# Kernel tuning notes

Hardware: AMD Instinct MI355X
Metric: run time of the kernel (lower is better)

The kernel has to match this reference:

```python
import jax, jax.numpy as jnp
import numpy as np

EPS = 1e-10
COMMITMENT_COST = 0.25


def setup_inputs() -> dict:
    key = jax.random.key(0)
    k1, k2 = jax.random.split(key)
    inputs = jax.random.normal(k1, (64, 64, 32, 32), dtype=jnp.float32)
    # nn.init.uniform_(weight, -1.0, 1.0)
    embeddings = jax.random.uniform(k2, (1024, 64), dtype=jnp.float32, minval=-1.0, maxval=1.0)
    return {"inputs": inputs, "embeddings": embeddings}


def reference(inputs, embeddings):
    B, C, H, W = inputs.shape  # C == embedding_dim
    K = embeddings.shape[0]
    x = jnp.transpose(inputs, (0, 2, 3, 1)).reshape(-1, C)  # [N, D]
    d = (jnp.sum(x * x, axis=1, keepdims=True)
         - 2.0 * (x @ embeddings.T)
         + jnp.sum(embeddings * embeddings, axis=1))  # [N, K]
    idx = jnp.argmin(d, axis=1)  # [N]
    # one-hot @ embeddings == gather
    q = jnp.take(embeddings, idx, axis=0)  # [N, D]
    x4 = x.reshape(B, H, W, C)
    q4 = q.reshape(B, H, W, C)
    e_latent = jnp.mean((jax.lax.stop_gradient(q4) - x4) ** 2)
    q_latent = jnp.mean((q4 - jax.lax.stop_gradient(x4)) ** 2)
    loss = q_latent + COMMITMENT_COST * e_latent
    # straight-through estimator
    st = x4 + jax.lax.stop_gradient(q4 - x4)
    # avg_probs = mean of one-hot encodings == normalized histogram
    n = idx.shape[0]
    avg_probs = jnp.zeros((K,), dtype=jnp.float32).at[idx].add(1.0) / n
    perplexity = jnp.exp(-jnp.sum(avg_probs * jnp.log(avg_probs + EPS)))
    quantized = jnp.transpose(st, (0, 3, 1, 2))
    return quantized, loss, perplexity
```

## Files before the change

kernel.cpp:

```cpp
#include <hip/hip_runtime.h>

#define N_TOTAL   65536
#define HW_SZ     1024
#define CDIM      64
#define K_CODES   1024
#define OUT_ELEMS 4194304
#define QT        256
#define NCHUNK    4
#define TAU       0.004f


typedef __attribute__((ext_vector_type(8))) short short8;
typedef __attribute__((ext_vector_type(4))) float f32x4;

__device__ __forceinline__ unsigned short f2bf(float x) {
    unsigned u = __float_as_uint(x);
    return (unsigned short)((u + 0x7FFFu + ((u >> 16) & 1u)) >> 16);
}
__device__ __forceinline__ float bf2f(unsigned short h) {
    return __uint_as_float(((unsigned)h) << 16);
}
__device__ __forceinline__ void gload_lds16(const void* g, void* l) {
    __builtin_amdgcn_global_load_lds(
        (const __attribute__((address_space(1))) void*)g,
        (__attribute__((address_space(3))) void*)l, 16, 0, 0);
}

__global__ void k_prep(const float* __restrict__ emb, float* __restrict__ enorm,
                       short* __restrict__ btab, unsigned int* __restrict__ hist) {
    int gid = blockIdx.x * 256 + threadIdx.x;
    int r  = gid >> 4;
    int d0 = (gid & 15) * 4;
    float4 v = *(const float4*)(emb + gid * 4);
    float s = v.x * v.x + v.y * v.y + v.z * v.z + v.w * v.w;
#pragma unroll
    for (int off = 1; off < 16; off <<= 1) s += __shfl_xor(s, off, 64);
    if ((gid & 15) == 0) enorm[r] = s;

    float vv[4] = {v.x, v.y, v.z, v.w};
    short h[4], l[4];
#pragma unroll
    for (int j = 0; j < 4; ++j) {
        unsigned short hh = f2bf(vv[j]);
        h[j] = (short)hh;
        l[j] = (short)f2bf(vv[j] - bf2f(hh));
    }
    int base = (r >> 4) * 2048 + (d0 >> 5) * 1024
             + ((((d0 >> 3) & 3) * 16 + (r & 15)) * 8) + (d0 & 7);
    *(short4*)&btab[base]       = make_short4(h[0], h[1], h[2], h[3]);
    *(short4*)&btab[base + 512] = make_short4(l[0], l[1], l[2], l[3]);

    if (gid < K_CODES) hist[gid] = 0u;
}

__global__ __launch_bounds__(1024, 1)
void k_argmin(const float* __restrict__ x, const float* __restrict__ emb,
              const short* __restrict__ btab, const float* __restrict__ enorm,
              unsigned int* __restrict__ hist, float* __restrict__ partials,
              float* __restrict__ out) {
    __shared__ __align__(16) short bufs[2][16 * 2048];
    __shared__ __align__(16) float ens[K_CODES];
    __shared__ float xnorm[QT];
    __shared__ float rd1[QT];
    __shared__ float rd2[QT];
    __shared__ int   ri[QT];
    __shared__ int   flist[QT];
    __shared__ __align__(16) float xqf[CDIM];
    __shared__ float wdd[16];
    __shared__ int   wii[16];
    __shared__ float spw[4];
    __shared__ int   nflag;
    float* tile = (float*)bufs;

    const int tid  = threadIdx.x;
    const int lane = tid & 63;
    const int w    = tid >> 6;
    const int quad = lane >> 4;
    const int col  = lane & 15;

    const int n0  = blockIdx.x * QT;
    const int b   = n0 >> 10;
    const int hw0 = n0 & 1023;

    auto stage_async = [&](int c, int bsel) {
        const short* src = btab + c * (16 * 2048);
#pragma unroll
        for (int i = 0; i < 4; ++i) {
            int idx = i * 1024 + tid;
            gload_lds16(&src[idx * 8], (void*)&bufs[bsel][idx * 8]);
        }
    };

    stage_async(0, 0);
    if (tid < 256) gload_lds16(&enorm[tid * 4], (void*)&ens[tid * 4]);

    const float* xb = x + b * (CDIM * HW_SZ) + hw0 + w * 16 + col;
    short8 afr[2][2];
    float nloc = 0.f;
#pragma unroll
    for (int kc = 0; kc < 2; ++kc) {
#pragma unroll
        for (int j = 0; j < 8; ++j) {
            int c0 = (kc * 4 + quad) * 8 + j;
            float v = xb[c0 * HW_SZ];
            unsigned short hh = f2bf(v);
            afr[kc][0][j] = (short)hh;
            afr[kc][1][j] = (short)f2bf(v - bf2f(hh));
            nloc = __builtin_fmaf(v, v, nloc);
        }
    }
    nloc += __shfl_xor(nloc, 16, 64);
    nloc += __shfl_xor(nloc, 32, 64);
    if (quad == 0) xnorm[w * 16 + col] = nloc;

    float d1[4], d2[4];
    int   i1[4];
#pragma unroll
    for (int t = 0; t < 4; ++t) { d1[t] = 3.4e38f; d2[t] = 3.4e38f; i1[t] = 0; }

    __syncthreads();

    for (int c = 0; c < NCHUNK; ++c) {
        if (c + 1 < NCHUNK) stage_async(c + 1, (c + 1) & 1);
        const short* bs = &bufs[c & 1][0];
        const int cbase = c * 256;

        short8 Ba[4], Bb[4];
        float  ena, enb;
        auto LDB = [&](short8 (&B)[4], float& en, int ctl) {
            const short* fp = bs + ctl * 2048 + lane * 8;
            B[0] = *(const short8*)(fp);
            B[1] = *(const short8*)(fp + 512);
            B[2] = *(const short8*)(fp + 1024);
            B[3] = *(const short8*)(fp + 1536);
            en   = ens[cbase + ctl * 16 + col];
        };
        auto COMP = [&](const short8 (&B)[4], float en, int mycode) {
            f32x4 a0 = {0.f, 0.f, 0.f, 0.f};
            f32x4 a1 = {0.f, 0.f, 0.f, 0.f};
            a0 = __builtin_amdgcn_mfma_f32_16x16x32_bf16(afr[0][1], B[0], a0, 0, 0, 0);
            a1 = __builtin_amdgcn_mfma_f32_16x16x32_bf16(afr[1][1], B[2], a1, 0, 0, 0);
            a0 = __builtin_amdgcn_mfma_f32_16x16x32_bf16(afr[0][0], B[1], a0, 0, 0, 0);
            a1 = __builtin_amdgcn_mfma_f32_16x16x32_bf16(afr[1][0], B[3], a1, 0, 0, 0);
            a0 = __builtin_amdgcn_mfma_f32_16x16x32_bf16(afr[0][0], B[0], a0, 0, 0, 0);
            a1 = __builtin_amdgcn_mfma_f32_16x16x32_bf16(afr[1][0], B[2], a1, 0, 0, 0);
#pragma unroll
            for (int reg = 0; reg < 4; ++reg) {
                float dot = a0[reg] + a1[reg];
                float d   = __builtin_fmaf(dot, -2.f, en);
                float d1o = d1[reg];
                d2[reg] = __builtin_amdgcn_fmed3f(d, d1o, d2[reg]);
                d1[reg] = fminf(d, d1o);
                i1[reg] = (d < d1o) ? mycode : i1[reg];
            }
        };

        LDB(Ba, ena, 0);
#pragma unroll
        for (int ctl = 0; ctl < 16; ctl += 2) {
            LDB(Bb, enb, ctl + 1);
            COMP(Ba, ena, cbase + ctl * 16 + col);
            if (ctl + 2 < 16) LDB(Ba, ena, ctl + 2);
            COMP(Bb, enb, cbase + (ctl + 1) * 16 + col);
        }
        __syncthreads();
    }

#pragma unroll
    for (int t = 0; t < 4; ++t) {
        float a1 = d1[t], a2 = d2[t];
        int ai = i1[t];
#pragma unroll
        for (int off = 1; off < 16; off <<= 1) {
            float o1 = __shfl_xor(a1, off, 64);
            float o2 = __shfl_xor(a2, off, 64);
            int   oi = __shfl_xor(ai, off, 64);
            if (o1 < a1 || (o1 == a1 && oi < ai)) {
                float loser = a1; a2 = fminf(fminf(a2, o2), loser); a1 = o1; ai = oi;
            } else {
                a2 = fminf(fminf(a2, o2), o1);
            }
        }
        d1[t] = a1; d2[t] = a2; i1[t] = ai;
    }

    if (tid == 0) nflag = 0;
    if (col == 0) {
#pragma unroll
        for (int reg = 0; reg < 4; ++reg) {
            int m = w * 16 + quad * 4 + reg;
            rd1[m] = d1[reg];
            rd2[m] = d2[reg];
            ri [m] = i1[reg];
        }
    }
    __syncthreads();

    if (tid < QT) {
        if (rd2[tid] - rd1[tid] < TAU) {
            int slot = atomicAdd(&nflag, 1);
            flist[slot] = tid;
        }
    }
    __syncthreads();

    for (int f = 0; f < nflag; ++f) {
        const int q = flist[f];
        if (tid < CDIM) xqf[tid] = x[b * (CDIM * HW_SZ) + tid * HW_SZ + hw0 + q];
        __syncthreads();
        const int k = tid;
        const float4* er = (const float4*)(emb + k * CDIM);
        const float4* xr = (const float4*)xqf;
        float dot = 0.f;
#pragma unroll 4
        for (int c4 = 0; c4 < 16; ++c4) {
            float4 e = er[c4], xv = xr[c4];
            dot += e.x * xv.x + e.y * xv.y + e.z * xv.z + e.w * xv.w;
        }
        float dm = ens[k] - 2.f * dot;
        int   im = k;
#pragma unroll
        for (int off = 1; off < 64; off <<= 1) {
            float od = __shfl_xor(dm, off, 64);
            int   oi = __shfl_xor(im, off, 64);
            if (od < dm || (od == dm && oi < im)) { dm = od; im = oi; }
        }
        if (lane == 0) { wdd[w] = dm; wii[w] = im; }
        __syncthreads();
        if (tid == 0) {
            float bd = wdd[0]; int bi = wii[0];
#pragma unroll
            for (int ww = 1; ww < 16; ++ww)
                if (wdd[ww] < bd || (wdd[ww] == bd && wii[ww] < bi)) { bd = wdd[ww]; bi = wii[ww]; }
            rd1[q] = bd; ri[q] = bi;
        }
        __syncthreads();
    }

    if (tid < QT) {
        int ai = ri[tid];
        atomicAdd(&hist[ai], 1u);
        float sp = rd1[tid] + xnorm[tid];
#pragma unroll
        for (int off = 32; off; off >>= 1) sp += __shfl_down(sp, off, 64);
        if (lane == 0) spw[tid >> 6] = sp;
    }
    __syncthreads();
    if (tid == 0) partials[blockIdx.x] = spw[0] + spw[1] + spw[2] + spw[3];

#pragma unroll
    for (int h = 0; h < 4; ++h) {
        {
            int q = tid >> 4, j4 = tid & 15;
            int code = ri[h * 64 + q];
            float4 e = *(const float4*)(emb + code * CDIM + j4 * 4);
            *(float4*)&tile[q * 73 + j4 * 4] = e;
        }
        __syncthreads();
        {
            int c = tid >> 4, s = tid & 15;
            int q = s * 4;
            float4 v;
            v.x = tile[(q + 0) * 73 + c];
            v.y = tile[(q + 1) * 73 + c];
            v.z = tile[(q + 2) * 73 + c];
            v.w = tile[(q + 3) * 73 + c];
            *(float4*)&out[b * (CDIM * HW_SZ) + c * HW_SZ + hw0 + h * 64 + q] = v;
        }
        if (h < 3) __syncthreads();
    }
}

__global__ void k_final(const float* __restrict__ partials,
                        const unsigned int* __restrict__ hist,
                        float* __restrict__ out) {
    int tid = threadIdx.x;
    float ss = partials[tid];
    float s = 0.f;
#pragma unroll
    for (int i = 0; i < 4; ++i) {
        float p = (float)hist[i * 256 + tid] * (1.0f / 65536.0f);
        s += p * logf(p + 1e-10f);
    }
    __shared__ float fin[8];
#pragma unroll
    for (int off = 32; off; off >>= 1) {
        ss += __shfl_down(ss, off, 64);
        s  += __shfl_down(s, off, 64);
    }
    if ((tid & 63) == 0) { fin[tid >> 6] = ss; fin[4 + (tid >> 6)] = s; }
    __syncthreads();
    if (tid == 0) {
        float sse = fin[0] + fin[1] + fin[2] + fin[3];
        float ent = fin[4] + fin[5] + fin[6] + fin[7];
        out[OUT_ELEMS]     = 1.25f * sse * (1.0f / (float)OUT_ELEMS);
        out[OUT_ELEMS + 1] = expf(-ent);
    }
}

extern "C" void kernel_launch(void* const* d_in, const int* in_sizes, int n_in,
                              void* d_out, int out_size, void* d_ws, size_t ws_size,
                              hipStream_t stream) {
    const float* x   = (const float*)d_in[0];
    const float* emb = (const float*)d_in[1];
    float* out = (float*)d_out;
    char* ws = (char*)d_ws;
    float*        enorm    = (float*)(ws);
    unsigned int* hist     = (unsigned int*)(ws + 4096);
    float*        partials = (float*)(ws + 8192);
    short*        btab     = (short*)(ws + 12288);

    k_prep  <<<64, 256, 0, stream>>>(emb, enorm, btab, hist);
    k_argmin<<<N_TOTAL / QT, 1024, 0, stream>>>(x, emb, btab, enorm, hist, partials, out);
    k_final <<<1, 256, 0, stream>>>(partials, hist, out);
}
```

Measured before the change: 153.9 us.

## Halve argmin block to 128 queries with 512 threads and two blocks per CU

Each argmin block now handles 128 query vectors with 512 threads instead of 256 with 1024. The codebook is streamed in 8 chunks of 128 codes so each block's LDS footprint halves and two blocks can co-reside per CU. The grid doubles to 512 blocks, which spreads work across the 256 CUs and lets one block's barriers and fallback loop overlap with another's compute. In exchange, each block re-streams the full codebook for fewer queries, doubling total codebook traffic, and the exact-recheck and output-transpose loops are re-indexed for the smaller block.

```diff
diff --git a/kernel.cpp b/kernel.cpp
--- a/kernel.cpp
+++ b/kernel.cpp
@@ -5,8 +5,8 @@
 #define CDIM      64
 #define K_CODES   1024
 #define OUT_ELEMS 4194304
-#define QT        256
-#define NCHUNK    4
+#define QT        128
+#define NCHUNK    8
 #define TAU       0.004f
 
 
@@ -53,12 +53,12 @@
     if (gid < K_CODES) hist[gid] = 0u;
 }
 
-__global__ __launch_bounds__(1024, 1)
+__global__ __launch_bounds__(512, 2)
 void k_argmin(const float* __restrict__ x, const float* __restrict__ emb,
               const short* __restrict__ btab, const float* __restrict__ enorm,
               unsigned int* __restrict__ hist, float* __restrict__ partials,
               float* __restrict__ out) {
-    __shared__ __align__(16) short bufs[2][16 * 2048];
+    __shared__ __align__(16) short bufs[2][8 * 2048];
     __shared__ __align__(16) float ens[K_CODES];
     __shared__ float xnorm[QT];
     __shared__ float rd1[QT];
@@ -66,9 +66,9 @@
     __shared__ int   ri[QT];
     __shared__ int   flist[QT];
     __shared__ __align__(16) float xqf[CDIM];
-    __shared__ float wdd[16];
-    __shared__ int   wii[16];
-    __shared__ float spw[4];
+    __shared__ float wdd[8];
+    __shared__ int   wii[8];
+    __shared__ float spw[2];
     __shared__ int   nflag;
     float* tile = (float*)bufs;
 
@@ -83,10 +83,10 @@
     const int hw0 = n0 & 1023;
 
     auto stage_async = [&](int c, int bsel) {
-        const short* src = btab + c * (16 * 2048);
+        const short* src = btab + c * (8 * 2048);
 #pragma unroll
         for (int i = 0; i < 4; ++i) {
-            int idx = i * 1024 + tid;
+            int idx = i * 512 + tid;
             gload_lds16(&src[idx * 8], (void*)&bufs[bsel][idx * 8]);
         }
     };
@@ -123,7 +123,7 @@
     for (int c = 0; c < NCHUNK; ++c) {
         if (c + 1 < NCHUNK) stage_async(c + 1, (c + 1) & 1);
         const short* bs = &bufs[c & 1][0];
-        const int cbase = c * 256;
+        const int cbase = c * 128;
 
         short8 Ba[4], Bb[4];
         float  ena, enb;
@@ -157,10 +157,10 @@
 
         LDB(Ba, ena, 0);
 #pragma unroll
-        for (int ctl = 0; ctl < 16; ctl += 2) {
+        for (int ctl = 0; ctl < 8; ctl += 2) {
             LDB(Bb, enb, ctl + 1);
             COMP(Ba, ena, cbase + ctl * 16 + col);
-            if (ctl + 2 < 16) LDB(Ba, ena, ctl + 2);
+            if (ctl + 2 < 8) LDB(Ba, ena, ctl + 2);
             COMP(Bb, enb, cbase + (ctl + 1) * 16 + col);
         }
         __syncthreads();
@@ -208,17 +208,20 @@
         const int q = flist[f];
         if (tid < CDIM) xqf[tid] = x[b * (CDIM * HW_SZ) + tid * HW_SZ + hw0 + q];
         __syncthreads();
-        const int k = tid;
-        const float4* er = (const float4*)(emb + k * CDIM);
-        const float4* xr = (const float4*)xqf;
-        float dot = 0.f;
+        float dm = 3.4e38f; int im = 0;
+        for (int cd = 0; cd < 2; ++cd) {
+            const int k = tid + cd * 512;
+            const float4* er = (const float4*)(emb + k * CDIM);
+            const float4* xr = (const float4*)xqf;
+            float dot = 0.f;
 #pragma unroll 4
-        for (int c4 = 0; c4 < 16; ++c4) {
-            float4 e = er[c4], xv = xr[c4];
-            dot += e.x * xv.x + e.y * xv.y + e.z * xv.z + e.w * xv.w;
-        }
-        float dm = ens[k] - 2.f * dot;
-        int   im = k;
+            for (int c4 = 0; c4 < 16; ++c4) {
+                float4 e = er[c4], xv = xr[c4];
+                dot += e.x * xv.x + e.y * xv.y + e.z * xv.z + e.w * xv.w;
+            }
+            float d = ens[k] - 2.f * dot;
+            if (d < dm) { dm = d; im = k; }
+        }
 #pragma unroll
         for (int off = 1; off < 64; off <<= 1) {
             float od = __shfl_xor(dm, off, 64);
@@ -230,7 +233,7 @@
         if (tid == 0) {
             float bd = wdd[0]; int bi = wii[0];
 #pragma unroll
-            for (int ww = 1; ww < 16; ++ww)
+            for (int ww = 1; ww < 8; ++ww)
                 if (wdd[ww] < bd || (wdd[ww] == bd && wii[ww] < bi)) { bd = wdd[ww]; bi = wii[ww]; }
             rd1[q] = bd; ri[q] = bi;
         }
@@ -246,28 +249,35 @@
         if (lane == 0) spw[tid >> 6] = sp;
     }
     __syncthreads();
-    if (tid == 0) partials[blockIdx.x] = spw[0] + spw[1] + spw[2] + spw[3];
-
-#pragma unroll
-    for (int h = 0; h < 4; ++h) {
+    if (tid == 0) partials[blockIdx.x] = spw[0] + spw[1];
+
+#pragma unroll
+    for (int h = 0; h < 2; ++h) {
         {
-            int q = tid >> 4, j4 = tid & 15;
+            int q = tid >> 3, j8 = tid & 7;
             int code = ri[h * 64 + q];
-            float4 e = *(const float4*)(emb + code * CDIM + j4 * 4);
-            *(float4*)&tile[q * 73 + j4 * 4] = e;
+            const float4* er = (const float4*)(emb + code * CDIM + j8 * 8);
+            float4 e0 = er[0], e1 = er[1];
+            float* dst = &tile[q * 73 + j8 * 8];
+            *(float4*)&dst[0] = e0;
+            *(float4*)&dst[4] = e1;
         }
         __syncthreads();
         {
-            int c = tid >> 4, s = tid & 15;
-            int q = s * 4;
-            float4 v;
-            v.x = tile[(q + 0) * 73 + c];
-            v.y = tile[(q + 1) * 73 + c];
-            v.z = tile[(q + 2) * 73 + c];
-            v.w = tile[(q + 3) * 73 + c];
-            *(float4*)&out[b * (CDIM * HW_SZ) + c * HW_SZ + hw0 + h * 64 + q] = v;
-        }
-        if (h < 3) __syncthreads();
+            int c = tid >> 3;
+            float* ob = out + b * (CDIM * HW_SZ) + c * HW_SZ + hw0 + h * 64;
+#pragma unroll
+            for (int p = 0; p < 2; ++p) {
+                int q = ((tid & 7) + p * 8) * 4;
+                float4 v;
+                v.x = tile[(q + 0) * 73 + c];
+                v.y = tile[(q + 1) * 73 + c];
+                v.z = tile[(q + 2) * 73 + c];
+                v.w = tile[(q + 3) * 73 + c];
+                *(float4*)&ob[q] = v;
+            }
+        }
+        if (h == 0) __syncthreads();
     }
 }
 
@@ -275,7 +285,7 @@
                         const unsigned int* __restrict__ hist,
                         float* __restrict__ out) {
     int tid = threadIdx.x;
-    float ss = partials[tid];
+    float ss = partials[tid] + partials[256 + tid];
     float s = 0.f;
 #pragma unroll
     for (int i = 0; i < 4; ++i) {
@@ -311,6 +321,6 @@
     short*        btab     = (short*)(ws + 12288);
 
     k_prep  <<<64, 256, 0, stream>>>(emb, enorm, btab, hist);
-    k_argmin<<<N_TOTAL / QT, 1024, 0, stream>>>(x, emb, btab, enorm, hist, partials, out);
+    k_argmin<<<N_TOTAL / QT, 512, 0, stream>>>(x, emb, btab, enorm, hist, partials, out);
     k_final <<<1, 256, 0, stream>>>(partials, hist, out);
 }
```

Measured after the change: 142.5 us. 7.4% less time.
